# Optimization experiments

Measured on AMD Instinct MI355X. Metric: run time of the kernel, lower is better.

The kernel has to match this reference:

```python
import jax, jax.numpy as jnp
import numpy as np

B, S, D, H = 2, 2048, 2048, 16
DEPTH = D // H


def setup_inputs() -> dict:
    key = jax.random.key(0)
    ks = jax.random.split(key, 12)
    std = 1.0 / np.sqrt(D)
    mk = lambda k, shape: (jax.random.uniform(k, shape, jnp.float32) * 2 - 1) * std
    # causal additive mask: 1.0 where future position (masked), 0.0 elsewhere
    mask = jnp.triu(jnp.ones((S, S), jnp.float32), k=1)[None, None]
    return {
        "q": jax.random.normal(ks[0], (B, S, D), jnp.float32),
        "k": jax.random.normal(ks[1], (B, S, D), jnp.float32),
        "v": jax.random.normal(ks[2], (B, S, D), jnp.float32),
        "mask": mask,
        "wq_w": mk(ks[3], (D, D)), "wq_b": mk(ks[4], (D,)),
        "wk_w": mk(ks[5], (D, D)), "wk_b": mk(ks[6], (D,)),
        "wv_w": mk(ks[7], (D, D)), "wv_b": mk(ks[8], (D,)),
        "dense_w": mk(ks[9], (D, D)), "dense_b": mk(ks[10], (D,)),
    }


def split_heads(x):
    # [B,S,D] -> [B,H,S,depth]
    b, s, _ = x.shape
    return x.reshape(b, s, H, DEPTH).transpose(0, 2, 1, 3)


def reference(q, k, v, mask, wq_w, wq_b, wk_w, wk_b, wv_w, wv_b, dense_w, dense_b):
    # torch Linear: y = x @ W.T + b
    qh = split_heads(q @ wq_w.T + wq_b)
    kh = split_heads(k @ wk_w.T + wk_b)
    vh = split_heads(v @ wv_w.T + wv_b)
    scale = 1.0 / jnp.sqrt(jnp.asarray(DEPTH, jnp.float32))
    logits = jnp.einsum("bhqd,bhkd->bhqk", qh, kh) * scale
    logits = logits + mask * (-1e9)
    weights = jax.nn.softmax(logits, axis=-1)  # dropout is identity in eval
    out = jnp.einsum("bhqk,bhkd->bhqd", weights, vh)
    out = out.transpose(0, 2, 1, 3).reshape(q.shape[0], -1, D)
    return out @ dense_w.T + dense_b
```

## Files before the change

kernel.cpp:

```cpp
#include <hip/hip_runtime.h>
#include <hip/hip_bf16.h>


typedef __bf16 bf16x8 __attribute__((ext_vector_type(8)));
typedef float f32x4 __attribute__((ext_vector_type(4)));
typedef float f32x16 __attribute__((ext_vector_type(16)));
typedef unsigned short u16;
typedef unsigned int u32;

#define DEV static __device__ __forceinline__

DEV void gload_lds16(const void* g, void* l) {
  __builtin_amdgcn_global_load_lds(
      (const __attribute__((address_space(1))) void*)g,
      (__attribute__((address_space(3))) void*)l, 16, 0, 0);
}

DEV f32x4 mfma16(bf16x8 a, bf16x8 b, f32x4 c) {
  return __builtin_amdgcn_mfma_f32_16x16x32_bf16(a, b, c, 0, 0, 0);
}

DEV f32x16 mfma32(bf16x8 a, bf16x8 b, f32x16 c) {
  return __builtin_amdgcn_mfma_f32_32x32x16_bf16(a, b, c, 0, 0, 0);
}

DEV u16 f2bf(float x) {
  return __builtin_bit_cast(u16, __float2bfloat16(x));
}

DEV u32 pack2(float lo, float hi_) {
  return (u32)f2bf(lo) | ((u32)f2bf(hi_) << 16);
}

#define BAR() __builtin_amdgcn_s_barrier()

__global__ void __launch_bounds__(256) conv_f32_bf16(
    const float* __restrict__ in, u16* __restrict__ out) {
  const size_t i = ((size_t)blockIdx.x * 256 + threadIdx.x) * 4;
  const float4 v = *reinterpret_cast<const float4*>(in + i);
  ushort4 o;
  o.x = f2bf(v.x); o.y = f2bf(v.y); o.z = f2bf(v.z); o.w = f2bf(v.w);
  *reinterpret_cast<ushort4*>(out + i) = o;
}

__global__ void __launch_bounds__(256) conv_all(
    const float* __restrict__ s0, const float* __restrict__ s1,
    const float* __restrict__ s2, const float* __restrict__ s3,
    const float* __restrict__ s4, const float* __restrict__ s5,
    const float* __restrict__ s6,
    u16* __restrict__ d0, u16* __restrict__ d1, u16* __restrict__ d2,
    u16* __restrict__ d3, u16* __restrict__ d4, u16* __restrict__ d5,
    u16* __restrict__ d6, const size_t nact, const size_t nw) {
  const int j = blockIdx.y;
  const size_t i = ((size_t)blockIdx.x * 256 + threadIdx.x) * 4;
  const float* s; u16* d; size_t n;
  switch (j) {
    case 0: s = s0; d = d0; n = nact; break;
    case 1: s = s1; d = d1; n = nact; break;
    case 2: s = s2; d = d2; n = nact; break;
    case 3: s = s3; d = d3; n = nw; break;
    case 4: s = s4; d = d4; n = nw; break;
    case 5: s = s5; d = d5; n = nw; break;
    default: s = s6; d = d6; n = nw; break;
  }
  if (i >= n) return;
  const float4 v = *reinterpret_cast<const float4*>(s + i);
  ushort4 o;
  o.x = f2bf(v.x); o.y = f2bf(v.y); o.z = f2bf(v.z); o.w = f2bf(v.w);
  *reinterpret_cast<ushort4*>(d + i) = o;
}

#define GK 2048

DEV void gemm256_core(const u16* __restrict__ A, const u16* __restrict__ Bw,
                      const float* __restrict__ bias, void* __restrict__ Cout,
                      const int m0, const int n0, const int N,
                      const int out_f32, u16* AsB, u16* BsB) {
  const int tid = threadIdx.x;
  const int lane = tid & 63;
  const int wid = tid >> 6;
  const int wr = wid >> 2, wc = wid & 3;
  const int g = lane >> 4;
  const int r16 = lane & 15;

  const int rp_h = tid >> 3;
  const int slot = (tid & 7) ^ (rp_h & 7);
  const int srow = rp_h * 2 + (slot >> 2);
  const int sch = slot & 3;
  const int aoff = (m0 + srow) * GK + sch * 8;
  const int boff = (n0 + srow) * GK + sch * 8;
  const int ldst = wid * 512;

#define STAGE_A(kt, hf) do {                                             \
    gload_lds16(A + (size_t)(aoff + (hf) * 262144 + (kt) * 64),          \
                AsB + (((kt)&1) * 2 + 0) * 8192 + (hf) * 4096 + ldst);   \
    gload_lds16(A + (size_t)(aoff + (hf) * 262144 + (kt) * 64 + 32),     \
                AsB + (((kt)&1) * 2 + 1) * 8192 + (hf) * 4096 + ldst);   \
  } while (0)
#define STAGE_B(kt, hf) do {                                             \
    gload_lds16(Bw + (size_t)(boff + (hf) * 262144 + (kt) * 64),         \
                BsB + (((kt)&1) * 2 + 0) * 8192 + (hf) * 4096 + ldst);   \
    gload_lds16(Bw + (size_t)(boff + (hf) * 262144 + (kt) * 64 + 32),    \
                BsB + (((kt)&1) * 2 + 1) * 8192 + (hf) * 4096 + ldst);   \
  } while (0)
#define READ_A(MH, buf, af) do {                                         \
    _Pragma("unroll") for (int i_ = 0; i_ < 4; ++i_) {                   \
      const int row_ = wr * 128 + (MH) * 64 + i_ * 16 + r16;             \
      const int rp_ = row_ >> 1;                                         \
      const int sl_ = (((row_ & 1) << 2) | g) ^ (rp_ & 7);               \
      const int off_ = rp_ * 64 + sl_ * 8;                               \
      af[i_][0] = *(const bf16x8*)(AsB + ((buf) * 2 + 0) * 8192 + off_); \
      af[i_][1] = *(const bf16x8*)(AsB + ((buf) * 2 + 1) * 8192 + off_); \
    } } while (0)
#define READ_B(NH, buf, bf) do {                                         \
    _Pragma("unroll") for (int j_ = 0; j_ < 2; ++j_) {                   \
      const int row_ = wc * 64 + (NH) * 32 + j_ * 16 + r16;              \
      const int rp_ = row_ >> 1;                                         \
      const int sl_ = (((row_ & 1) << 2) | g) ^ (rp_ & 7);               \
      const int off_ = rp_ * 64 + sl_ * 8;                               \
      bf[j_][0] = *(const bf16x8*)(BsB + ((buf) * 2 + 0) * 8192 + off_); \
      bf[j_][1] = *(const bf16x8*)(BsB + ((buf) * 2 + 1) * 8192 + off_); \
    } } while (0)
#define MFMA_Q(MH, NH, af, bf) do {                                      \
    __builtin_amdgcn_s_setprio(1);                                       \
    _Pragma("unroll") for (int i_ = 0; i_ < 4; ++i_)                     \
    _Pragma("unroll") for (int j_ = 0; j_ < 2; ++j_) {                   \
      acc[(MH) * 4 + i_][(NH) * 2 + j_] =                                \
          mfma16(af[i_][0], bf[j_][0], acc[(MH) * 4 + i_][(NH) * 2 + j_]); \
      acc[(MH) * 4 + i_][(NH) * 2 + j_] =                                \
          mfma16(af[i_][1], bf[j_][1], acc[(MH) * 4 + i_][(NH) * 2 + j_]); \
    }                                                                    \
    __builtin_amdgcn_s_setprio(0);                                       \
  } while (0)

  f32x4 acc[8][4];
#pragma unroll
  for (int i = 0; i < 8; ++i)
#pragma unroll
    for (int j = 0; j < 4; ++j) acc[i][j] = {0.f, 0.f, 0.f, 0.f};

  STAGE_B(0, 0); STAGE_B(0, 1); STAGE_A(0, 0); STAGE_A(0, 1);
  STAGE_B(1, 0); STAGE_B(1, 1);
  asm volatile("s_waitcnt vmcnt(4)" ::: "memory");
  BAR();

  for (int it = 0; it < 16; ++it) {
    const bool tail = (it == 15);
    const int t0 = 2 * it, t1 = t0 + 1;
    bf16x8 af[4][2], bf0[2][2], bf1[2][2];
    READ_A(0, 0, af); READ_B(0, 0, bf0);
    STAGE_A(t1, 0);
    BAR(); MFMA_Q(0, 0, af, bf0); BAR();
    READ_B(1, 0, bf1);
    STAGE_A(t1, 1);
    BAR(); MFMA_Q(0, 1, af, bf1); BAR();
    READ_A(1, 0, af);
    if (!tail) STAGE_B(t0 + 2, 0);
    BAR(); MFMA_Q(1, 0, af, bf0); BAR();
    if (!tail) STAGE_B(t0 + 2, 1);
    BAR(); MFMA_Q(1, 1, af, bf1); BAR();
    READ_A(0, 1, af); READ_B(0, 1, bf0);
    if (!tail) {
      STAGE_A(t0 + 2, 0);
      asm volatile("s_waitcnt vmcnt(6)" ::: "memory");
    } else {
      asm volatile("s_waitcnt vmcnt(0)" ::: "memory");
    }
    BAR(); MFMA_Q(0, 0, af, bf0); BAR();
    READ_B(1, 1, bf1);
    if (!tail) STAGE_A(t0 + 2, 1);
    BAR(); MFMA_Q(0, 1, af, bf1); BAR();
    READ_A(1, 1, af);
    if (!tail) STAGE_B(t1 + 2, 0);
    BAR(); MFMA_Q(1, 0, af, bf0); BAR();
    if (!tail) {
      STAGE_B(t1 + 2, 1);
      asm volatile("s_waitcnt vmcnt(4)" ::: "memory");
    } else {
      asm volatile("s_waitcnt vmcnt(0)" ::: "memory");
    }
    BAR(); MFMA_Q(1, 1, af, bf1); BAR();
  }

  const int rbase = m0 + wr * 128 + g * 4;
  const int cb = n0 + wc * 64 + r16;
#pragma unroll
  for (int i = 0; i < 8; ++i) {
#pragma unroll
    for (int j = 0; j < 4; ++j) {
      const int c = cb + j * 16;
      const float bv = bias[c];
#pragma unroll
      for (int r = 0; r < 4; ++r) {
        const float v = acc[i][j][r] + bv;
        const size_t idx = (size_t)(rbase + i * 16 + r) * N + c;
        if (out_f32) ((float*)Cout)[idx] = v;
        else ((u16*)Cout)[idx] = f2bf(v);
      }
    }
  }
#undef STAGE_A
#undef STAGE_B
#undef READ_A
#undef READ_B
#undef MFMA_Q
}

__global__ void __launch_bounds__(512, 2) gemm_qkv3(
    const u16* __restrict__ A0, const u16* __restrict__ A1,
    const u16* __restrict__ A2, const u16* __restrict__ W0,
    const u16* __restrict__ W1, const u16* __restrict__ W2,
    const float* __restrict__ b0, const float* __restrict__ b1,
    const float* __restrict__ b2, u16* __restrict__ C0,
    u16* __restrict__ C1, u16* __restrict__ C2) {
  __shared__ u16 AsB[4 * 8192];
  __shared__ u16 BsB[4 * 8192];
  const int logical = (blockIdx.x & 7) * 48 + (blockIdx.x >> 3);
  const int which = logical >> 7;
  const int inner = logical & 127;
  const int m0 = (inner & 15) * 256;
  const int n0 = (inner >> 4) * 256;
  const u16* A = which == 0 ? A0 : which == 1 ? A1 : A2;
  const u16* W = which == 0 ? W0 : which == 1 ? W1 : W2;
  const float* bb = which == 0 ? b0 : which == 1 ? b1 : b2;
  u16* C = which == 0 ? C0 : which == 1 ? C1 : C2;
  gemm256_core(A, W, bb, C, m0, n0, 2048, 0, AsB, BsB);
}

__global__ void __launch_bounds__(512, 2) gemm_one(
    const u16* __restrict__ A, const u16* __restrict__ Bw,
    const float* __restrict__ bias, void* __restrict__ Cout,
    const int out_f32) {
  __shared__ u16 AsB[4 * 8192];
  __shared__ u16 BsB[4 * 8192];
  const int logical = (blockIdx.x & 7) * 16 + (blockIdx.x >> 3);
  const int m0 = (logical & 15) * 256;
  const int n0 = (logical >> 4) * 256;
  gemm256_core(A, Bw, bias, Cout, m0, n0, 2048, out_f32, AsB, BsB);
}

#define SEQ 2048
#define DMODEL 2048
#define DH 128
#define QBLK 128
#define KBLK 64
#define C1 0.12751744f
#define THR_RAW 62.73f

__global__ void __launch_bounds__(256, 2) flash_attn(
    const u16* __restrict__ Qh, const u16* __restrict__ Kh,
    const u16* __restrict__ Vh, u16* __restrict__ O) {
  __shared__ u16 Ks[KBLK * DH];
  __shared__ u16 Vt[DH * KBLK];

  const int tid = threadIdx.x;
  const int lane = tid & 63;
  const int w = tid >> 6;
  const int hi = lane >> 5;
  const int l31 = lane & 31;

  const int cc = blockIdx.x;
  const int low = cc & 15;
  const int bh = (cc >> 4) & 31;
  const int h = bh & 15;
  const int b = bh >> 4;
  const int g0 = low ^ h;
  const int qt = b ? (15 - g0) : g0;
  const int q0 = qt * QBLK;
  const size_t rowbase = (size_t)b * SEQ;
  const int hoff = h * DH;
  const int qw = q0 + w * 32;
  const int qlane = qw + l31;

  bf16x8 aq[8];
  {
    const u16* qp = &Qh[(rowbase + qlane) * DMODEL + hoff + hi * 8];
#pragma unroll
    for (int c = 0; c < 8; ++c)
      aq[c] = *reinterpret_cast<const bf16x8*>(qp + c * 16);
  }

  f32x16 oacc[4];
#pragma unroll
  for (int dt = 0; dt < 4; ++dt)
#pragma unroll
    for (int r = 0; r < 16; ++r) oacc[dt][r] = 0.f;
  float mrow = -1e30f, lrow = 0.f;

  const int krl = w * 16 + (lane >> 4);
  const int kg4 = w * 4 + (lane >> 4);
  const int du = lane & 15;

  const int nkt = 2 * qt + 2;
  const int ktd = qw >> 6;

  uint4 vv[4];
#pragma unroll
  for (int r = 0; r < 4; ++r)
    vv[r] = *reinterpret_cast<const uint4*>(
        &Vh[(rowbase + kg4 * 4 + r) * DMODEL + hoff + du * 8]);

  for (int kt = 0; kt < nkt; ++kt) {
    const int k0 = kt * KBLK;
    __syncthreads();

#pragma unroll
    for (int i = 0; i < 4; ++i) {
      const int r = krl + i * 4;
      const int cg = (lane & 15) ^ (r & 15);
      gload_lds16(&Kh[(rowbase + k0 + r) * DMODEL + hoff + cg * 8],
                  &Ks[(w * 16 + i * 4) * DH]);
    }

#pragma unroll
    for (int j = 0; j < 8; ++j) {
      const int d = du * 8 + j;
      ushort4 pk4;
      pk4.x = ((const u16*)&vv[0])[j];
      pk4.y = ((const u16*)&vv[1])[j];
      pk4.z = ((const u16*)&vv[2])[j];
      pk4.w = ((const u16*)&vv[3])[j];
      const int slot = (((kg4 >> 1) ^ ((d >> 2) & 7)) * 8) + (kg4 & 1) * 4;
      *reinterpret_cast<ushort4*>(&Vt[d * KBLK + slot]) = pk4;
    }

    __syncthreads();

    if (kt + 1 < nkt) {
#pragma unroll
      for (int r = 0; r < 4; ++r)
        vv[r] = *reinterpret_cast<const uint4*>(
            &Vh[(rowbase + k0 + KBLK + kg4 * 4 + r) * DMODEL + hoff + du * 8]);
    }

    if (kt > ktd) continue;

    const bool diag = (kt == ktd);
    const bool act1 = (kt < ktd) || (w & 1);
    const bool m0q = diag && !(w & 1);
    const bool m1q = diag && (w & 1);

    float p[2][16];
    {
      f32x16 s;
#pragma unroll
      for (int r = 0; r < 16; ++r) s[r] = 0.f;
      __builtin_amdgcn_s_setprio(1);
#pragma unroll
      for (int c = 0; c < 8; ++c) {
        const int row = l31;
        const bf16x8 kf = *reinterpret_cast<const bf16x8*>(
            &Ks[row * DH + (((c * 2 + hi) ^ (row & 15)) * 8)]);
        s = mfma32(kf, aq[c], s);
      }
      __builtin_amdgcn_s_setprio(0);
#pragma unroll
      for (int r = 0; r < 16; ++r) {
        const int krow = (r & 3) + 8 * (r >> 2) + 4 * hi;
        p[0][r] = (m0q && (k0 + krow > qlane)) ? -1e9f : s[r];
      }
    }
    if (act1) {
      f32x16 s;
#pragma unroll
      for (int r = 0; r < 16; ++r) s[r] = 0.f;
      __builtin_amdgcn_s_setprio(1);
#pragma unroll
      for (int c = 0; c < 8; ++c) {
        const int row = 32 + l31;
        const bf16x8 kf = *reinterpret_cast<const bf16x8*>(
            &Ks[row * DH + (((c * 2 + hi) ^ (row & 15)) * 8)]);
        s = mfma32(kf, aq[c], s);
      }
      __builtin_amdgcn_s_setprio(0);
#pragma unroll
      for (int r = 0; r < 16; ++r) {
        const int krow = (r & 3) + 8 * (r >> 2) + 4 * hi;
        p[1][r] = (m1q && (k0 + 32 + krow > qlane)) ? -1e9f : s[r];
      }
    } else {
#pragma unroll
      for (int r = 0; r < 16; ++r) p[1][r] = -1e9f;
    }

    float mx = fmaxf(p[0][0], p[0][1]);
#pragma unroll
    for (int r = 2; r < 16; ++r) mx = fmaxf(mx, p[0][r]);
#pragma unroll
    for (int r = 0; r < 16; ++r) mx = fmaxf(mx, p[1][r]);
    mx = fmaxf(mx, __shfl_xor(mx, 32));

    const bool need = (mx > mrow + THR_RAW);
    if (__any((int)need)) {
      const float mn = fmaxf(mrow, mx);
      const float al = exp2f((mrow - mn) * C1);
      mrow = mn;
      lrow *= al;
#pragma unroll
      for (int r = 0; r < 16; ++r) {
        const float ar = __shfl(al, (r & 3) + 8 * (r >> 2) + 4 * hi);
#pragma unroll
        for (int dt = 0; dt < 4; ++dt) oacc[dt][r] *= ar;
      }
    }

    float sum = 0.f;
#pragma unroll
    for (int t = 0; t < 2; ++t)
#pragma unroll
      for (int r = 0; r < 16; ++r) {
        p[t][r] = exp2f((p[t][r] - mrow) * C1);
        sum += p[t][r];
      }
    sum += __shfl_xor(sum, 32);
    lrow += sum;

    u32 pk[2][8];
#pragma unroll
    for (int t = 0; t < 2; ++t)
#pragma unroll
      for (int m = 0; m < 8; ++m)
        pk[t][m] = pack2(p[t][2 * m], p[t][2 * m + 1]);

    __builtin_amdgcn_s_setprio(1);
#pragma unroll
    for (int ks = 0; ks < 4; ++ks) {
      if (ks >= 2 && !act1) break;
      const int t = ks >> 1;
      const int bs = (ks & 1) * 4;
      const u32 s0 = __shfl_xor(pk[t][bs + 0], 32);
      const u32 s1 = __shfl_xor(pk[t][bs + 1], 32);
      const u32 s2 = __shfl_xor(pk[t][bs + 2], 32);
      const u32 s3 = __shfl_xor(pk[t][bs + 3], 32);
      union { u32 u[4]; bf16x8 v; } pa;
      pa.u[0] = hi ? s2 : pk[t][bs + 0];
      pa.u[1] = hi ? s3 : pk[t][bs + 1];
      pa.u[2] = hi ? pk[t][bs + 2] : s0;
      pa.u[3] = hi ? pk[t][bs + 3] : s1;
#pragma unroll
      for (int dt = 0; dt < 4; ++dt) {
        const int d = dt * 32 + l31;
        const bf16x8 vf = *reinterpret_cast<const bf16x8*>(
            &Vt[d * KBLK + (((ks * 2 + hi) ^ ((d >> 2) & 7)) * 8)]);
        oacc[dt] = mfma32(pa.v, vf, oacc[dt]);
      }
    }
    __builtin_amdgcn_s_setprio(0);
  }

  const float li = __builtin_amdgcn_rcpf(lrow);
#pragma unroll
  for (int r = 0; r < 16; ++r) {
    const int rowq = (r & 3) + 8 * (r >> 2) + 4 * hi;
    const float lr = __shfl(li, rowq);
    u16* op = &O[(rowbase + qw + rowq) * DMODEL + hoff + l31];
#pragma unroll
    for (int dt = 0; dt < 4; ++dt) op[dt * 32] = f2bf(oacc[dt][r] * lr);
  }
}

extern "C" void kernel_launch(void* const* d_in, const int* in_sizes, int n_in,
                              void* d_out, int out_size, void* d_ws,
                              size_t ws_size, hipStream_t stream) {
  const int Bv = 2, S = 2048, D = 2048;
  const int M = Bv * S;
  const size_t NT = (size_t)M * D;
  const size_t NW = (size_t)D * D;

  const float* q = (const float*)d_in[0];
  const float* k = (const float*)d_in[1];
  const float* v = (const float*)d_in[2];
  const float* wq_w = (const float*)d_in[4];
  const float* wq_b = (const float*)d_in[5];
  const float* wk_w = (const float*)d_in[6];
  const float* wk_b = (const float*)d_in[7];
  const float* wv_w = (const float*)d_in[8];
  const float* wv_b = (const float*)d_in[9];
  const float* dw = (const float*)d_in[10];
  const float* db = (const float*)d_in[11];
  float* out = (float*)d_out;

  const dim3 blk(256);
  const dim3 gblk(512);
  const dim3 gattn(512);
  const size_t need = (7 * NT + 4 * NW) * 2;

  if (ws_size >= need) {
    u16* base = (u16*)d_ws;
    u16* Xq = base;
    u16* Xk = Xq + NT;
    u16* Xv = Xk + NT;
    u16* Wq = Xv + NT;
    u16* Wk = Wq + NW;
    u16* Wv = Wk + NW;
    u16* Wd = Wv + NW;
    u16* Qh = Wd + NW;
    u16* Kh = Qh + NT;
    u16* Vh = Kh + NT;
    u16* Obf = Vh + NT;

    conv_all<<<dim3((unsigned)(NT / 1024), 7), blk, 0, stream>>>(
        q, k, v, wq_w, wk_w, wv_w, dw, Xq, Xk, Xv, Wq, Wk, Wv, Wd, NT, NW);
    gemm_qkv3<<<dim3(384), gblk, 0, stream>>>(
        Xq, Xk, Xv, Wq, Wk, Wv, wq_b, wk_b, wv_b, Qh, Kh, Vh);
    flash_attn<<<gattn, blk, 0, stream>>>(Qh, Kh, Vh, Obf);
    gemm_one<<<dim3(128), gblk, 0, stream>>>(Obf, Wd, db, out, 1);
  } else {
    u16* Xbf = (u16*)d_ws;
    u16* Wbf = Xbf + NT;
    u16* Qh = Wbf + NW;
    u16* Kh = Qh + NT;
    u16* Vh = Kh + NT;
    u16* Obf = Vh + NT;
    const dim3 gact((unsigned)(NT / 1024));
    const dim3 gw((unsigned)(NW / 1024));

    conv_f32_bf16<<<gact, blk, 0, stream>>>(q, Xbf);
    conv_f32_bf16<<<gw, blk, 0, stream>>>(wq_w, Wbf);
    gemm_one<<<dim3(128), gblk, 0, stream>>>(Xbf, Wbf, wq_b, Qh, 0);
    conv_f32_bf16<<<gact, blk, 0, stream>>>(k, Xbf);
    conv_f32_bf16<<<gw, blk, 0, stream>>>(wk_w, Wbf);
    gemm_one<<<dim3(128), gblk, 0, stream>>>(Xbf, Wbf, wk_b, Kh, 0);
    conv_f32_bf16<<<gact, blk, 0, stream>>>(v, Xbf);
    conv_f32_bf16<<<gw, blk, 0, stream>>>(wv_w, Wbf);
    gemm_one<<<dim3(128), gblk, 0, stream>>>(Xbf, Wbf, wv_b, Vh, 0);
    flash_attn<<<gattn, blk, 0, stream>>>(Qh, Kh, Vh, Obf);
    conv_f32_bf16<<<gw, blk, 0, stream>>>(dw, Wbf);
    gemm_one<<<dim3(128), gblk, 0, stream>>>(Obf, Wbf, db, out, 1);
  }
}
```

Before: 344.4 us.

## Shrink GEMM tiles to 128x128 and double-buffer K tiles in flash attention

```diff
diff --git a/kernel.cpp b/kernel.cpp
--- a/kernel.cpp
+++ b/kernel.cpp
@@ -72,72 +72,79 @@
 
 #define GK 2048
 
-DEV void gemm256_core(const u16* __restrict__ A, const u16* __restrict__ Bw,
+DEV void gemm128_core(const u16* __restrict__ A, const u16* __restrict__ Bw,
                       const float* __restrict__ bias, void* __restrict__ Cout,
                       const int m0, const int n0, const int N,
                       const int out_f32, u16* AsB, u16* BsB) {
   const int tid = threadIdx.x;
   const int lane = tid & 63;
   const int wid = tid >> 6;
-  const int wr = wid >> 2, wc = wid & 3;
+  const int wr = wid >> 1, wc = wid & 1;
   const int g = lane >> 4;
   const int r16 = lane & 15;
 
-  const int rp_h = tid >> 3;
-  const int slot = (tid & 7) ^ (rp_h & 7);
-  const int srow = rp_h * 2 + (slot >> 2);
-  const int sch = slot & 3;
-  const int aoff = (m0 + srow) * GK + sch * 8;
-  const int boff = (n0 + srow) * GK + sch * 8;
-  const int ldst = wid * 512;
-
-#define STAGE_A(kt, hf) do {                                             \
-    gload_lds16(A + (size_t)(aoff + (hf) * 262144 + (kt) * 64),          \
-                AsB + (((kt)&1) * 2 + 0) * 8192 + (hf) * 4096 + ldst);   \
-    gload_lds16(A + (size_t)(aoff + (hf) * 262144 + (kt) * 64 + 32),     \
-                AsB + (((kt)&1) * 2 + 1) * 8192 + (hf) * 4096 + ldst);   \
+  int offA[2], offB[2], dstE[2];
+#pragma unroll
+  for (int rr = 0; rr < 2; ++rr) {
+    const int G = rr * 256 + tid;
+    const int rp = G >> 3;
+    const int s = (G & 7) ^ (rp & 7);
+    const int row = rp * 2 + (s >> 2);
+    const int ch = s & 3;
+    offA[rr] = (m0 + row) * GK + ch * 8;
+    offB[rr] = (n0 + row) * GK + ch * 8;
+    dstE[rr] = rr * 2048 + wid * 512;
+  }
+
+#define STAGE_A(kt, kh) do {                                              \
+    u16* base_ = AsB + (((kt) & 1) * 2 + (kh)) * 4096;                    \
+    const int go_ = (kt) * 64 + (kh) * 32;                                \
+    gload_lds16(A + (size_t)(offA[0] + go_), base_ + dstE[0]);            \
+    gload_lds16(A + (size_t)(offA[1] + go_), base_ + dstE[1]);            \
   } while (0)
-#define STAGE_B(kt, hf) do {                                             \
-    gload_lds16(Bw + (size_t)(boff + (hf) * 262144 + (kt) * 64),         \
-                BsB + (((kt)&1) * 2 + 0) * 8192 + (hf) * 4096 + ldst);   \
-    gload_lds16(Bw + (size_t)(boff + (hf) * 262144 + (kt) * 64 + 32),    \
-                BsB + (((kt)&1) * 2 + 1) * 8192 + (hf) * 4096 + ldst);   \
+#define STAGE_B(kt, kh) do {                                              \
+    u16* base_ = BsB + (((kt) & 1) * 2 + (kh)) * 4096;                    \
+    const int go_ = (kt) * 64 + (kh) * 32;                                \
+    gload_lds16(Bw + (size_t)(offB[0] + go_), base_ + dstE[0]);           \
+    gload_lds16(Bw + (size_t)(offB[1] + go_), base_ + dstE[1]);           \
   } while (0)
-#define READ_A(MH, buf, af) do {                                         \
-    _Pragma("unroll") for (int i_ = 0; i_ < 4; ++i_) {                   \
-      const int row_ = wr * 128 + (MH) * 64 + i_ * 16 + r16;             \
-      const int rp_ = row_ >> 1;                                         \
-      const int sl_ = (((row_ & 1) << 2) | g) ^ (rp_ & 7);               \
-      const int off_ = rp_ * 64 + sl_ * 8;                               \
-      af[i_][0] = *(const bf16x8*)(AsB + ((buf) * 2 + 0) * 8192 + off_); \
-      af[i_][1] = *(const bf16x8*)(AsB + ((buf) * 2 + 1) * 8192 + off_); \
+#define READ_A(MH, buf) do {                                              \
+    _Pragma("unroll") for (int i_ = 0; i_ < 2; ++i_) {                    \
+      const int row_ = wr * 64 + ((MH) * 2 + i_) * 16 + r16;              \
+      const int rp_ = row_ >> 1;                                          \
+      const int sl_ = (((row_ & 1) << 2) | g) ^ (rp_ & 7);                \
+      const int off_ = rp_ * 64 + sl_ * 8;                                \
+      af[i_][0] = *(const bf16x8*)(AsB + ((buf) * 2 + 0) * 4096 + off_);  \
+      af[i_][1] = *(const bf16x8*)(AsB + ((buf) * 2 + 1) * 4096 + off_);  \
     } } while (0)
-#define READ_B(NH, buf, bf) do {                                         \
-    _Pragma("unroll") for (int j_ = 0; j_ < 2; ++j_) {                   \
-      const int row_ = wc * 64 + (NH) * 32 + j_ * 16 + r16;              \
-      const int rp_ = row_ >> 1;                                         \
-      const int sl_ = (((row_ & 1) << 2) | g) ^ (rp_ & 7);               \
-      const int off_ = rp_ * 64 + sl_ * 8;                               \
-      bf[j_][0] = *(const bf16x8*)(BsB + ((buf) * 2 + 0) * 8192 + off_); \
-      bf[j_][1] = *(const bf16x8*)(BsB + ((buf) * 2 + 1) * 8192 + off_); \
+#define READ_B(NH, buf, bf) do {                                          \
+    _Pragma("unroll") for (int j_ = 0; j_ < 2; ++j_) {                    \
+      const int row_ = wc * 64 + ((NH) * 2 + j_) * 16 + r16;              \
+      const int rp_ = row_ >> 1;                                          \
+      const int sl_ = (((row_ & 1) << 2) | g) ^ (rp_ & 7);                \
+      const int off_ = rp_ * 64 + sl_ * 8;                                \
+      bf[j_][0] = *(const bf16x8*)(BsB + ((buf) * 2 + 0) * 4096 + off_);  \
+      bf[j_][1] = *(const bf16x8*)(BsB + ((buf) * 2 + 1) * 4096 + off_);  \
     } } while (0)
-#define MFMA_Q(MH, NH, af, bf) do {                                      \
-    __builtin_amdgcn_s_setprio(1);                                       \
-    _Pragma("unroll") for (int i_ = 0; i_ < 4; ++i_)                     \
-    _Pragma("unroll") for (int j_ = 0; j_ < 2; ++j_) {                   \
-      acc[(MH) * 4 + i_][(NH) * 2 + j_] =                                \
-          mfma16(af[i_][0], bf[j_][0], acc[(MH) * 4 + i_][(NH) * 2 + j_]); \
-      acc[(MH) * 4 + i_][(NH) * 2 + j_] =                                \
-          mfma16(af[i_][1], bf[j_][1], acc[(MH) * 4 + i_][(NH) * 2 + j_]); \
-    }                                                                    \
-    __builtin_amdgcn_s_setprio(0);                                       \
+#define MFMA_Q(MH, NH, bf) do {                                           \
+    __builtin_amdgcn_s_setprio(1);                                        \
+    _Pragma("unroll") for (int i_ = 0; i_ < 2; ++i_)                      \
+    _Pragma("unroll") for (int j_ = 0; j_ < 2; ++j_) {                    \
+      f32x4 c_ = acc[(MH) * 2 + i_][(NH) * 2 + j_];                       \
+      c_ = mfma16(af[i_][0], bf[j_][0], c_);                              \
+      c_ = mfma16(af[i_][1], bf[j_][1], c_);                              \
+      acc[(MH) * 2 + i_][(NH) * 2 + j_] = c_;                             \
+    }                                                                     \
+    __builtin_amdgcn_s_setprio(0);                                        \
   } while (0)
 
-  f32x4 acc[8][4];
-#pragma unroll
-  for (int i = 0; i < 8; ++i)
+  f32x4 acc[4][4];
+#pragma unroll
+  for (int i = 0; i < 4; ++i)
 #pragma unroll
     for (int j = 0; j < 4; ++j) acc[i][j] = {0.f, 0.f, 0.f, 0.f};
+
+  bf16x8 af[2][2], bf0[2][2], bf1[2][2];
 
   STAGE_B(0, 0); STAGE_B(0, 1); STAGE_A(0, 0); STAGE_A(0, 1);
   STAGE_B(1, 0); STAGE_B(1, 1);
@@ -147,45 +154,44 @@
   for (int it = 0; it < 16; ++it) {
     const bool tail = (it == 15);
     const int t0 = 2 * it, t1 = t0 + 1;
-    bf16x8 af[4][2], bf0[2][2], bf1[2][2];
-    READ_A(0, 0, af); READ_B(0, 0, bf0);
+    READ_A(0, 0); READ_B(0, 0, bf0);
     STAGE_A(t1, 0);
-    BAR(); MFMA_Q(0, 0, af, bf0); BAR();
+    BAR(); MFMA_Q(0, 0, bf0); BAR();
     READ_B(1, 0, bf1);
     STAGE_A(t1, 1);
-    BAR(); MFMA_Q(0, 1, af, bf1); BAR();
-    READ_A(1, 0, af);
+    BAR(); MFMA_Q(0, 1, bf1); BAR();
+    READ_A(1, 0);
     if (!tail) STAGE_B(t0 + 2, 0);
-    BAR(); MFMA_Q(1, 0, af, bf0); BAR();
+    BAR(); MFMA_Q(1, 0, bf0); BAR();
     if (!tail) STAGE_B(t0 + 2, 1);
-    BAR(); MFMA_Q(1, 1, af, bf1); BAR();
-    READ_A(0, 1, af); READ_B(0, 1, bf0);
+    BAR(); MFMA_Q(1, 1, bf1); BAR();
+    READ_A(0, 1); READ_B(0, 1, bf0);
     if (!tail) {
       STAGE_A(t0 + 2, 0);
       asm volatile("s_waitcnt vmcnt(6)" ::: "memory");
     } else {
       asm volatile("s_waitcnt vmcnt(0)" ::: "memory");
     }
-    BAR(); MFMA_Q(0, 0, af, bf0); BAR();
+    BAR(); MFMA_Q(0, 0, bf0); BAR();
     READ_B(1, 1, bf1);
     if (!tail) STAGE_A(t0 + 2, 1);
-    BAR(); MFMA_Q(0, 1, af, bf1); BAR();
-    READ_A(1, 1, af);
+    BAR(); MFMA_Q(0, 1, bf1); BAR();
+    READ_A(1, 1);
     if (!tail) STAGE_B(t1 + 2, 0);
-    BAR(); MFMA_Q(1, 0, af, bf0); BAR();
+    BAR(); MFMA_Q(1, 0, bf0); BAR();
     if (!tail) {
       STAGE_B(t1 + 2, 1);
       asm volatile("s_waitcnt vmcnt(4)" ::: "memory");
     } else {
       asm volatile("s_waitcnt vmcnt(0)" ::: "memory");
     }
-    BAR(); MFMA_Q(1, 1, af, bf1); BAR();
-  }
-
-  const int rbase = m0 + wr * 128 + g * 4;
+    BAR(); MFMA_Q(1, 1, bf1); BAR();
+  }
+
+  const int rbase = m0 + wr * 64 + g * 4;
   const int cb = n0 + wc * 64 + r16;
 #pragma unroll
-  for (int i = 0; i < 8; ++i) {
+  for (int i = 0; i < 4; ++i) {
 #pragma unroll
     for (int j = 0; j < 4; ++j) {
       const int c = cb + j * 16;
@@ -206,37 +212,37 @@
 #undef MFMA_Q
 }
 
-__global__ void __launch_bounds__(512, 2) gemm_qkv3(
+__global__ void __launch_bounds__(256, 2) gemm_qkv3(
     const u16* __restrict__ A0, const u16* __restrict__ A1,
     const u16* __restrict__ A2, const u16* __restrict__ W0,
     const u16* __restrict__ W1, const u16* __restrict__ W2,
     const float* __restrict__ b0, const float* __restrict__ b1,
     const float* __restrict__ b2, u16* __restrict__ C0,
     u16* __restrict__ C1, u16* __restrict__ C2) {
-  __shared__ u16 AsB[4 * 8192];
-  __shared__ u16 BsB[4 * 8192];
-  const int logical = (blockIdx.x & 7) * 48 + (blockIdx.x >> 3);
-  const int which = logical >> 7;
-  const int inner = logical & 127;
-  const int m0 = (inner & 15) * 256;
-  const int n0 = (inner >> 4) * 256;
+  __shared__ u16 AsB[4 * 4096];
+  __shared__ u16 BsB[4 * 4096];
+  const int logical = (blockIdx.x & 7) * 192 + (blockIdx.x >> 3);
+  const int which = logical >> 9;
+  const int inner = logical & 511;
+  const int m0 = (inner & 31) << 7;
+  const int n0 = (inner >> 5) << 7;
   const u16* A = which == 0 ? A0 : which == 1 ? A1 : A2;
   const u16* W = which == 0 ? W0 : which == 1 ? W1 : W2;
   const float* bb = which == 0 ? b0 : which == 1 ? b1 : b2;
   u16* C = which == 0 ? C0 : which == 1 ? C1 : C2;
-  gemm256_core(A, W, bb, C, m0, n0, 2048, 0, AsB, BsB);
-}
-
-__global__ void __launch_bounds__(512, 2) gemm_one(
+  gemm128_core(A, W, bb, C, m0, n0, 2048, 0, AsB, BsB);
+}
+
+__global__ void __launch_bounds__(256, 2) gemm_one(
     const u16* __restrict__ A, const u16* __restrict__ Bw,
     const float* __restrict__ bias, void* __restrict__ Cout,
     const int out_f32) {
-  __shared__ u16 AsB[4 * 8192];
-  __shared__ u16 BsB[4 * 8192];
-  const int logical = (blockIdx.x & 7) * 16 + (blockIdx.x >> 3);
-  const int m0 = (logical & 15) * 256;
-  const int n0 = (logical >> 4) * 256;
-  gemm256_core(A, Bw, bias, Cout, m0, n0, 2048, out_f32, AsB, BsB);
+  __shared__ u16 AsB[4 * 4096];
+  __shared__ u16 BsB[4 * 4096];
+  const int logical = (blockIdx.x & 7) * 64 + (blockIdx.x >> 3);
+  const int m0 = (logical & 31) << 7;
+  const int n0 = (logical >> 5) << 7;
+  gemm128_core(A, Bw, bias, Cout, m0, n0, 2048, out_f32, AsB, BsB);
 }
 
 #define SEQ 2048
@@ -250,7 +256,7 @@
 __global__ void __launch_bounds__(256, 2) flash_attn(
     const u16* __restrict__ Qh, const u16* __restrict__ Kh,
     const u16* __restrict__ Vh, u16* __restrict__ O) {
-  __shared__ u16 Ks[KBLK * DH];
+  __shared__ u16 Ks[2][KBLK * DH];
   __shared__ u16 Vt[DH * KBLK];
 
   const int tid = threadIdx.x;
@@ -294,6 +300,17 @@
   const int nkt = 2 * qt + 2;
   const int ktd = qw >> 6;
 
+  auto stageK = [&](int kt) {
+#pragma unroll
+    for (int i = 0; i < 4; ++i) {
+      const int r = krl + i * 4;
+      const int cg = (lane & 15) ^ (r & 15);
+      gload_lds16(&Kh[(rowbase + kt * KBLK + r) * DMODEL + hoff + cg * 8],
+                  &Ks[kt & 1][(w * 16 + i * 4) * DH]);
+    }
+  };
+
+  stageK(0);
   uint4 vv[4];
 #pragma unroll
   for (int r = 0; r < 4; ++r)
@@ -302,14 +319,11 @@
 
   for (int kt = 0; kt < nkt; ++kt) {
     const int k0 = kt * KBLK;
-    __syncthreads();
-
-#pragma unroll
-    for (int i = 0; i < 4; ++i) {
-      const int r = krl + i * 4;
-      const int cg = (lane & 15) ^ (r & 15);
-      gload_lds16(&Kh[(rowbase + k0 + r) * DMODEL + hoff + cg * 8],
-                  &Ks[(w * 16 + i * 4) * DH]);
+    if (kt + 1 < nkt) {
+      stageK(kt + 1);
+      asm volatile("s_waitcnt vmcnt(4)" ::: "memory");
+    } else {
+      asm volatile("s_waitcnt vmcnt(0)" ::: "memory");
     }
 
 #pragma unroll
@@ -323,8 +337,61 @@
       const int slot = (((kg4 >> 1) ^ ((d >> 2) & 7)) * 8) + (kg4 & 1) * 4;
       *reinterpret_cast<ushort4*>(&Vt[d * KBLK + slot]) = pk4;
     }
-
-    __syncthreads();
+    asm volatile("s_waitcnt lgkmcnt(0)" ::: "memory");
+    BAR();
+
+    const bool active = (kt <= ktd);
+    const u16* kb = &Ks[kt & 1][0];
+    float p[2][16];
+    bool act1 = false;
+
+    if (active) {
+      const bool diag = (kt == ktd);
+      act1 = (kt < ktd) || (w & 1);
+      const bool m0q = diag && !(w & 1);
+      const bool m1q = diag && (w & 1);
+      {
+        f32x16 s;
+#pragma unroll
+        for (int r = 0; r < 16; ++r) s[r] = 0.f;
+        __builtin_amdgcn_s_setprio(1);
+#pragma unroll
+        for (int c = 0; c < 8; ++c) {
+          const int row = l31;
+          const bf16x8 kf = *reinterpret_cast<const bf16x8*>(
+              &kb[row * DH + (((c * 2 + hi) ^ (row & 15)) * 8)]);
+          s = mfma32(kf, aq[c], s);
+        }
+        __builtin_amdgcn_s_setprio(0);
+#pragma unroll
+        for (int r = 0; r < 16; ++r) {
+          const int krow = (r & 3) + 8 * (r >> 2) + 4 * hi;
+          p[0][r] = (m0q && (k0 + krow > qlane)) ? -1e9f : s[r];
+        }
+      }
+      if (act1) {
+        f32x16 s;
+#pragma unroll
+        for (int r = 0; r < 16; ++r) s[r] = 0.f;
+        __builtin_amdgcn_s_setprio(1);
+#pragma unroll
+        for (int c = 0; c < 8; ++c) {
+          const int row = 32 + l31;
+          const bf16x8 kf = *reinterpret_cast<const bf16x8*>(
+              &kb[row * DH + (((c * 2 + hi) ^ (row & 15)) * 8)]);
+          s = mfma32(kf, aq[c], s);
+        }
+        __builtin_amdgcn_s_setprio(0);
+#pragma unroll
+        for (int r = 0; r < 16; ++r) {
+          const int krow = (r & 3) + 8 * (r >> 2) + 4 * hi;
+          p[1][r] = (m1q && (k0 + 32 + krow > qlane)) ? -1e9f : s[r];
+        }
+      } else {
+#pragma unroll
+        for (int r = 0; r < 16; ++r) p[1][r] = -1e9f;
+      }
+    }
 
     if (kt + 1 < nkt) {
 #pragma unroll
@@ -333,119 +400,73 @@
             &Vh[(rowbase + k0 + KBLK + kg4 * 4 + r) * DMODEL + hoff + du * 8]);
     }
 
-    if (kt > ktd) continue;
-
-    const bool diag = (kt == ktd);
-    const bool act1 = (kt < ktd) || (w & 1);
-    const bool m0q = diag && !(w & 1);
-    const bool m1q = diag && (w & 1);
-
-    float p[2][16];
-    {
-      f32x16 s;
-#pragma unroll
-      for (int r = 0; r < 16; ++r) s[r] = 0.f;
+    if (active) {
+      float mx = fmaxf(p[0][0], p[0][1]);
+#pragma unroll
+      for (int r = 2; r < 16; ++r) mx = fmaxf(mx, p[0][r]);
+#pragma unroll
+      for (int r = 0; r < 16; ++r) mx = fmaxf(mx, p[1][r]);
+      mx = fmaxf(mx, __shfl_xor(mx, 32));
+
+      const bool need = (mx > mrow + THR_RAW);
+      if (__any((int)need)) {
+        const float mn = fmaxf(mrow, mx);
+        const float al = exp2f((mrow - mn) * C1);
+        mrow = mn;
+        lrow *= al;
+#pragma unroll
+        for (int r = 0; r < 16; ++r) {
+          const float ar = __shfl(al, (r & 3) + 8 * (r >> 2) + 4 * hi);
+#pragma unroll
+          for (int dt = 0; dt < 4; ++dt) oacc[dt][r] *= ar;
+        }
+      }
+
+      float sum = 0.f;
+#pragma unroll
+      for (int t = 0; t < 2; ++t)
+#pragma unroll
+        for (int r = 0; r < 16; ++r) {
+          p[t][r] = exp2f((p[t][r] - mrow) * C1);
+          sum += p[t][r];
+        }
+      sum += __shfl_xor(sum, 32);
+      lrow += sum;
+
+      u32 pk[2][8];
+#pragma unroll
+      for (int t = 0; t < 2; ++t)
+#pragma unroll
+        for (int m = 0; m < 8; ++m)
+          pk[t][m] = pack2(p[t][2 * m], p[t][2 * m + 1]);
+
       __builtin_amdgcn_s_setprio(1);
 #pragma unroll
-      for (int c = 0; c < 8; ++c) {
-        const int row = l31;
-        const bf16x8 kf = *reinterpret_cast<const bf16x8*>(
-            &Ks[row * DH + (((c * 2 + hi) ^ (row & 15)) * 8)]);
-        s = mfma32(kf, aq[c], s);
+      for (int ks = 0; ks < 4; ++ks) {
+        if (ks >= 2 && !act1) break;
+        const int t = ks >> 1;
+        const int bs = (ks & 1) * 4;
+        const u32 s0 = __shfl_xor(pk[t][bs + 0], 32);
+        const u32 s1 = __shfl_xor(pk[t][bs + 1], 32);
+        const u32 s2 = __shfl_xor(pk[t][bs + 2], 32);
+        const u32 s3 = __shfl_xor(pk[t][bs + 3], 32);
+        union { u32 u[4]; bf16x8 v; } pa;
+        pa.u[0] = hi ? s2 : pk[t][bs + 0];
+        pa.u[1] = hi ? s3 : pk[t][bs + 1];
+        pa.u[2] = hi ? pk[t][bs + 2] : s0;
+        pa.u[3] = hi ? pk[t][bs + 3] : s1;
+#pragma unroll
+        for (int dt = 0; dt < 4; ++dt) {
+          const int d = dt * 32 + l31;
+          const bf16x8 vf = *reinterpret_cast<const bf16x8*>(
+              &Vt[d * KBLK + (((ks * 2 + hi) ^ ((d >> 2) & 7)) * 8)]);
+          oacc[dt] = mfma32(pa.v, vf, oacc[dt]);
+        }
       }
       __builtin_amdgcn_s_setprio(0);
-#pragma unroll
-      for (int r = 0; r < 16; ++r) {
-        const int krow = (r & 3) + 8 * (r >> 2) + 4 * hi;
-        p[0][r] = (m0q && (k0 + krow > qlane)) ? -1e9f : s[r];
-      }
-    }
-    if (act1) {
-      f32x16 s;
-#pragma unroll
-      for (int r = 0; r < 16; ++r) s[r] = 0.f;
-      __builtin_amdgcn_s_setprio(1);
-#pragma unroll
-      for (int c = 0; c < 8; ++c) {
-        const int row = 32 + l31;
-        const bf16x8 kf = *reinterpret_cast<const bf16x8*>(
-            &Ks[row * DH + (((c * 2 + hi) ^ (row & 15)) * 8)]);
-        s = mfma32(kf, aq[c], s);
-      }
-      __builtin_amdgcn_s_setprio(0);
-#pragma unroll
-      for (int r = 0; r < 16; ++r) {
-        const int krow = (r & 3) + 8 * (r >> 2) + 4 * hi;
-        p[1][r] = (m1q && (k0 + 32 + krow > qlane)) ? -1e9f : s[r];
-      }
-    } else {
-#pragma unroll
-      for (int r = 0; r < 16; ++r) p[1][r] = -1e9f;
-    }
-
-    float mx = fmaxf(p[0][0], p[0][1]);
-#pragma unroll
-    for (int r = 2; r < 16; ++r) mx = fmaxf(mx, p[0][r]);
-#pragma unroll
-    for (int r = 0; r < 16; ++r) mx = fmaxf(mx, p[1][r]);
-    mx = fmaxf(mx, __shfl_xor(mx, 32));
-
-    const bool need = (mx > mrow + THR_RAW);
-    if (__any((int)need)) {
-      const float mn = fmaxf(mrow, mx);
-      const float al = exp2f((mrow - mn) * C1);
-      mrow = mn;
-      lrow *= al;
-#pragma unroll
-      for (int r = 0; r < 16; ++r) {
-        const float ar = __shfl(al, (r & 3) + 8 * (r >> 2) + 4 * hi);
-#pragma unroll
-        for (int dt = 0; dt < 4; ++dt) oacc[dt][r] *= ar;
-      }
-    }
-
-    float sum = 0.f;
-#pragma unroll
-    for (int t = 0; t < 2; ++t)
-#pragma unroll
-      for (int r = 0; r < 16; ++r) {
-        p[t][r] = exp2f((p[t][r] - mrow) * C1);
-        sum += p[t][r];
-      }
-    sum += __shfl_xor(sum, 32);
-    lrow += sum;
-
-    u32 pk[2][8];
-#pragma unroll
-    for (int t = 0; t < 2; ++t)
-#pragma unroll
-      for (int m = 0; m < 8; ++m)
-        pk[t][m] = pack2(p[t][2 * m], p[t][2 * m + 1]);
-
-    __builtin_amdgcn_s_setprio(1);
-#pragma unroll
-    for (int ks = 0; ks < 4; ++ks) {
-      if (ks >= 2 && !act1) break;
-      const int t = ks >> 1;
-      const int bs = (ks & 1) * 4;
-      const u32 s0 = __shfl_xor(pk[t][bs + 0], 32);
-      const u32 s1 = __shfl_xor(pk[t][bs + 1], 32);
-      const u32 s2 = __shfl_xor(pk[t][bs + 2], 32);
-      const u32 s3 = __shfl_xor(pk[t][bs + 3], 32);
-      union { u32 u[4]; bf16x8 v; } pa;
-      pa.u[0] = hi ? s2 : pk[t][bs + 0];
-      pa.u[1] = hi ? s3 : pk[t][bs + 1];
-      pa.u[2] = hi ? pk[t][bs + 2] : s0;
-      pa.u[3] = hi ? pk[t][bs + 3] : s1;
-#pragma unroll
-      for (int dt = 0; dt < 4; ++dt) {
-        const int d = dt * 32 + l31;
-        const bf16x8 vf = *reinterpret_cast<const bf16x8*>(
-            &Vt[d * KBLK + (((ks * 2 + hi) ^ ((d >> 2) & 7)) * 8)]);
-        oacc[dt] = mfma32(pa.v, vf, oacc[dt]);
-      }
-    }
-    __builtin_amdgcn_s_setprio(0);
+    }
+
+    BAR();
   }
 
   const float li = __builtin_amdgcn_rcpf(lrow);
@@ -481,7 +502,6 @@
   float* out = (float*)d_out;
 
   const dim3 blk(256);
-  const dim3 gblk(512);
   const dim3 gattn(512);
   const size_t need = (7 * NT + 4 * NW) * 2;
 
@@ -501,10 +521,10 @@
 
     conv_all<<<dim3((unsigned)(NT / 1024), 7), blk, 0, stream>>>(
         q, k, v, wq_w, wk_w, wv_w, dw, Xq, Xk, Xv, Wq, Wk, Wv, Wd, NT, NW);
-    gemm_qkv3<<<dim3(384), gblk, 0, stream>>>(
+    gemm_qkv3<<<dim3(1536), blk, 0, stream>>>(
         Xq, Xk, Xv, Wq, Wk, Wv, wq_b, wk_b, wv_b, Qh, Kh, Vh);
     flash_attn<<<gattn, blk, 0, stream>>>(Qh, Kh, Vh, Obf);
-    gemm_one<<<dim3(128), gblk, 0, stream>>>(Obf, Wd, db, out, 1);
+    gemm_one<<<dim3(512), blk, 0, stream>>>(Obf, Wd, db, out, 1);
   } else {
     u16* Xbf = (u16*)d_ws;
     u16* Wbf = Xbf + NT;
@@ -517,15 +537,15 @@
 
     conv_f32_bf16<<<gact, blk, 0, stream>>>(q, Xbf);
     conv_f32_bf16<<<gw, blk, 0, stream>>>(wq_w, Wbf);
-    gemm_one<<<dim3(128), gblk, 0, stream>>>(Xbf, Wbf, wq_b, Qh, 0);
+    gemm_one<<<dim3(512), blk, 0, stream>>>(Xbf, Wbf, wq_b, Qh, 0);
     conv_f32_bf16<<<gact, blk, 0, stream>>>(k, Xbf);
     conv_f32_bf16<<<gw, blk, 0, stream>>>(wk_w, Wbf);
-    gemm_one<<<dim3(128), gblk, 0, stream>>>(Xbf, Wbf, wk_b, Kh, 0);
+    gemm_one<<<dim3(512), blk, 0, stream>>>(Xbf, Wbf, wk_b, Kh, 0);
     conv_f32_bf16<<<gact, blk, 0, stream>>>(v, Xbf);
     conv_f32_bf16<<<gw, blk, 0, stream>>>(wv_w, Wbf);
-    gemm_one<<<dim3(128), gblk, 0, stream>>>(Xbf, Wbf, wv_b, Vh, 0);
+    gemm_one<<<dim3(512), blk, 0, stream>>>(Xbf, Wbf, wv_b, Vh, 0);
     flash_attn<<<gattn, blk, 0, stream>>>(Qh, Kh, Vh, Obf);
     conv_f32_bf16<<<gw, blk, 0, stream>>>(dw, Wbf);
-    gemm_one<<<dim3(128), gblk, 0, stream>>>(Obf, Wbf, db, out, 1);
-  }
-}
+    gemm_one<<<dim3(512), blk, 0, stream>>>(Obf, Wbf, db, out, 1);
+  }
+}
```

Result: faster. 322.5 us (median of 2 runs) (-6.4%).
